# Optimization experiments

Measured on AMD Instinct MI355X. Metric: run time of the kernel, lower is better.

## Reference

```python
import jax, jax.numpy as jnp
import numpy as np

IN_F = 1024
OUT_F = 4096
BATCH = 1024

def setup_inputs() -> dict:
    key = jax.random.key(0)
    k1, k2, k3, k4 = jax.random.split(key, 4)
    s = np.sqrt(IN_F).astype(np.float32)  # weight init range, as in reset_parameters
    x = jax.random.normal(k1, (BATCH, IN_F), dtype=jnp.float32)
    weights = jax.random.uniform(k2, (OUT_F, IN_F), minval=-s, maxval=s, dtype=jnp.float32)
    centers = 0.1 * jax.random.normal(k3, (OUT_F, IN_F), dtype=jnp.float32)
    # sigmas ~ U(in-0.5, in+0.5); inv_covar = 1/sigmas
    sigmas = jax.random.uniform(k4, (OUT_F, IN_F), minval=IN_F - 0.5, maxval=IN_F + 0.5, dtype=jnp.float32)
    inv_covar = 1.0 / sigmas
    return {"x": x, "weights": weights, "centers": centers, "inv_covar": inv_covar}

def reference(x, weights, centers, inv_covar):
    # linear part with FGN bias: b_i = -sum_j W_ij * C_ij
    biases = -jnp.sum(weights * centers, axis=-1)  # (O,)
    l = x @ weights.T + biases                      # (B, O)
    # diag Mahalanobis: g_bi = sum_j (x_bj - c_ij)^2 * ic_ij^2
    # expanded to GEMMs to avoid the (B, O, I) broadcast intermediate
    ic2 = inv_covar * inv_covar                     # (O, I)
    g = ((x * x) @ ic2.T
         - 2.0 * (x @ (centers * ic2).T)
         + jnp.sum(centers * centers * ic2, axis=-1))  # (B, O)
    return l * jnp.exp(-g)
```

## Files before the change

### kernel.cpp

```cpp
#include <hip/hip_runtime.h>
#include <hip/hip_bf16.h>
#include <stdint.h>


typedef __attribute__((ext_vector_type(8))) __bf16 bf16x8;
typedef __attribute__((ext_vector_type(16))) float f32x16;

__device__ __forceinline__ unsigned short f2bf(float f) {
  union { float f; unsigned int u; } v; v.f = f;
  unsigned int u = v.u;
  unsigned int r = (u + 0x7FFFu + ((u >> 16) & 1u)) >> 16;
  return (unsigned short)r;
}

__global__ __launch_bounds__(256) void prep(
    const float* __restrict__ X, const float* __restrict__ W,
    const float* __restrict__ C, const float* __restrict__ IC,
    unsigned short* __restrict__ Wb, unsigned short* __restrict__ I2b,
    unsigned short* __restrict__ M2b,
    unsigned short* __restrict__ Xb, unsigned short* __restrict__ Qb,
    float* __restrict__ bias, float* __restrict__ dvec) {
  const int b = blockIdx.x;
  if (b < 1024) {
    const int wave = threadIdx.x >> 6;
    const int lane = threadIdx.x & 63;
    const int row  = b * 4 + wave;
    const float4* W4 = (const float4*)W + (size_t)row * 256;
    const float4* C4 = (const float4*)C + (size_t)row * 256;
    const float4* I4 = (const float4*)IC + (size_t)row * 256;
    ushort4* Wo = (ushort4*)Wb + (size_t)row * 256;
    ushort4* Io = (ushort4*)I2b + (size_t)row * 256;
    ushort4* Mo = (ushort4*)M2b + (size_t)row * 256;
    float swc = 0.f, sd = 0.f;
#pragma unroll
    for (int p = 0; p < 4; ++p) {
      int idx = lane + p * 64;
      float4 w = W4[idx], c = C4[idx], ic = I4[idx];
      float i2x = ic.x * ic.x, i2y = ic.y * ic.y, i2z = ic.z * ic.z, i2w = ic.w * ic.w;
      swc += w.x * c.x + w.y * c.y + w.z * c.z + w.w * c.w;
      sd  += c.x * c.x * i2x + c.y * c.y * i2y + c.z * c.z * i2z + c.w * c.w * i2w;
      ushort4 a, bb, m;
      a.x = f2bf(w.x); a.y = f2bf(w.y); a.z = f2bf(w.z); a.w = f2bf(w.w);
      bb.x = f2bf(i2x); bb.y = f2bf(i2y); bb.z = f2bf(i2z); bb.w = f2bf(i2w);
      m.x = f2bf(-2.f * c.x * i2x); m.y = f2bf(-2.f * c.y * i2y);
      m.z = f2bf(-2.f * c.z * i2z); m.w = f2bf(-2.f * c.w * i2w);
      Wo[idx] = a; Io[idx] = bb; Mo[idx] = m;
    }
#pragma unroll
    for (int off = 32; off > 0; off >>= 1) {
      swc += __shfl_down(swc, off);
      sd  += __shfl_down(sd, off);
    }
    if (lane == 0) { bias[row] = -swc; dvec[row] = sd; }
  } else {
    const int xb = b - 1024;
#pragma unroll
    for (int j = 0; j < 4; ++j) {
      int idx = xb * 1024 + j * 256 + threadIdx.x;
      float4 v = ((const float4*)X)[idx];
      ushort4 a, q;
      a.x = f2bf(v.x); a.y = f2bf(v.y); a.z = f2bf(v.z); a.w = f2bf(v.w);
      q.x = f2bf(v.x * v.x); q.y = f2bf(v.y * v.y);
      q.z = f2bf(v.z * v.z); q.w = f2bf(v.w * v.w);
      ((ushort4*)Xb)[idx] = a;
      ((ushort4*)Qb)[idx] = q;
    }
  }
}

#define GLD16(gp, lp)                                                          \
  __builtin_amdgcn_global_load_lds(                                            \
      (const __attribute__((address_space(1))) unsigned int*)(gp),             \
      (__attribute__((address_space(3))) unsigned int*)(lp), 16, 0, 0)

__global__ __launch_bounds__(256, 1) void fgn_gemm(
    const unsigned short* __restrict__ Xb, const unsigned short* __restrict__ Qb,
    const unsigned short* __restrict__ Wb, const unsigned short* __restrict__ I2b,
    const unsigned short* __restrict__ M2b,
    const float* __restrict__ bias, const float* __restrict__ dvec,
    float* __restrict__ out) {
  __shared__ unsigned short lds[2][5][4096];
  const int t = threadIdx.x;
  const int m0 = blockIdx.y * 128;
  const int n0 = blockIdx.x * 128;

  const int srow = t >> 2;
  const int gco  = ((t & 3) ^ ((t >> 3) & 3)) * 8;

  const unsigned short* g0 = Xb  + (size_t)(m0 + srow) * 1024 + gco;
  const unsigned short* g1 = Qb  + (size_t)(m0 + srow) * 1024 + gco;
  const unsigned short* g2 = Wb  + (size_t)(n0 + srow) * 1024 + gco;
  const unsigned short* g3 = I2b + (size_t)(n0 + srow) * 1024 + gco;
  const unsigned short* g4 = M2b + (size_t)(n0 + srow) * 1024 + gco;

#define STAGE(B, S)                                                            \
  do {                                                                         \
    const int ko = (S) * 32;                                                   \
    GLD16(g0 + ko,         &lds[B][0][t * 8]);                                 \
    GLD16(g0 + ko + 65536, &lds[B][0][2048 + t * 8]);                          \
    GLD16(g1 + ko,         &lds[B][1][t * 8]);                                 \
    GLD16(g1 + ko + 65536, &lds[B][1][2048 + t * 8]);                          \
    GLD16(g2 + ko,         &lds[B][2][t * 8]);                                 \
    GLD16(g2 + ko + 65536, &lds[B][2][2048 + t * 8]);                          \
    GLD16(g3 + ko,         &lds[B][3][t * 8]);                                 \
    GLD16(g3 + ko + 65536, &lds[B][3][2048 + t * 8]);                          \
    GLD16(g4 + ko,         &lds[B][4][t * 8]);                                 \
    GLD16(g4 + ko + 65536, &lds[B][4][2048 + t * 8]);                          \
  } while (0)

  const int wave = t >> 6, lane = t & 63;
  const int wx = wave & 1, wy = wave >> 1;
  const int ln = lane & 31, kh = lane >> 5;
  const int sw = (ln >> 1) & 3;

  int aoff[2], boff[2];
#pragma unroll
  for (int i = 0; i < 2; ++i) {
    aoff[i] = (wy * 64 + i * 32 + ln) * 32;
    boff[i] = (wx * 64 + i * 32 + ln) * 32;
  }

  f32x16 accL[2][2], accG[2][2];
#pragma unroll
  for (int i = 0; i < 2; ++i)
#pragma unroll
    for (int j = 0; j < 2; ++j) { accL[i][j] = (f32x16)0.f; accG[i][j] = (f32x16)0.f; }

#define COMPUTE(B)                                                             \
  do {                                                                         \
    _Pragma("unroll")                                                          \
    for (int ks = 0; ks < 2; ++ks) {                                           \
      const int co = ((ks * 2 + kh) ^ sw) * 8;                                 \
      bf16x8 ax[2], aq[2], bw[2], bi[2], bm[2];                                \
      _Pragma("unroll")                                                        \
      for (int i = 0; i < 2; ++i) {                                            \
        ax[i] = *(const bf16x8*)&lds[B][0][aoff[i] + co];                      \
        aq[i] = *(const bf16x8*)&lds[B][1][aoff[i] + co];                      \
        bw[i] = *(const bf16x8*)&lds[B][2][boff[i] + co];                      \
        bi[i] = *(const bf16x8*)&lds[B][3][boff[i] + co];                      \
        bm[i] = *(const bf16x8*)&lds[B][4][boff[i] + co];                      \
      }                                                                        \
      _Pragma("unroll")                                                        \
      for (int mt = 0; mt < 2; ++mt)                                           \
        _Pragma("unroll")                                                      \
        for (int nt = 0; nt < 2; ++nt) {                                       \
          accL[mt][nt] = __builtin_amdgcn_mfma_f32_32x32x16_bf16(              \
              ax[mt], bw[nt], accL[mt][nt], 0, 0, 0);                          \
          accG[mt][nt] = __builtin_amdgcn_mfma_f32_32x32x16_bf16(              \
              aq[mt], bi[nt], accG[mt][nt], 0, 0, 0);                          \
          accG[mt][nt] = __builtin_amdgcn_mfma_f32_32x32x16_bf16(              \
              ax[mt], bm[nt], accG[mt][nt], 0, 0, 0);                          \
        }                                                                      \
    }                                                                          \
  } while (0)

  STAGE(0, 0);
  __syncthreads();
#pragma unroll 1
  for (int p = 0; p < 16; ++p) {
    STAGE(1, 2 * p + 1);
    COMPUTE(0);
    __syncthreads();
    if (p < 15) STAGE(0, 2 * p + 2);
    COMPUTE(1);
    __syncthreads();
  }

#pragma unroll
  for (int nt = 0; nt < 2; ++nt) {
    int col = n0 + wx * 64 + nt * 32 + ln;
    float bn = bias[col], dn = dvec[col];
#pragma unroll
    for (int mt = 0; mt < 2; ++mt) {
      int rb = m0 + wy * 64 + mt * 32 + 4 * kh;
#pragma unroll
      for (int r = 0; r < 16; ++r) {
        int row = rb + (r & 3) + 8 * (r >> 2);
        float l  = accL[mt][nt][r] + bn;
        float gg = accG[mt][nt][r] + dn;
        out[(size_t)row * 4096 + col] = l * __expf(-gg);
      }
    }
  }
#undef STAGE
#undef COMPUTE
}

extern "C" void kernel_launch(void* const* d_in, const int* in_sizes, int n_in,
                              void* d_out, int out_size, void* d_ws, size_t ws_size,
                              hipStream_t stream) {
  const float* x  = (const float*)d_in[0];
  const float* W  = (const float*)d_in[1];
  const float* C  = (const float*)d_in[2];
  const float* IC = (const float*)d_in[3];
  float* out = (float*)d_out;

  char* ws = (char*)d_ws;
  unsigned short* Wb  = (unsigned short*)(ws);
  unsigned short* I2b = (unsigned short*)(ws + (8u << 20));
  unsigned short* M2b = (unsigned short*)(ws + (16u << 20));
  unsigned short* Xb  = (unsigned short*)(ws + (24u << 20));
  unsigned short* Qb  = (unsigned short*)(ws + (26u << 20));
  float* bias = (float*)(ws + (28u << 20));
  float* dvec = (float*)(ws + (28u << 20) + 16384);

  hipLaunchKernelGGL(prep, dim3(1280), dim3(256), 0, stream, x, W, C, IC,
                     Wb, I2b, M2b, Xb, Qb, bias, dvec);
  hipLaunchKernelGGL(fgn_gemm, dim3(32, 8), dim3(256), 0, stream,
                     Xb, Qb, Wb, I2b, M2b, bias, dvec, out);
}
```

Baseline: 138.3 us.

## Split K across wave groups, compute x² in-kernel, drop Q buffer

```diff
diff --git a/kernel.cpp b/kernel.cpp
--- a/kernel.cpp
+++ b/kernel.cpp
@@ -17,8 +17,7 @@
     const float* __restrict__ X, const float* __restrict__ W,
     const float* __restrict__ C, const float* __restrict__ IC,
     unsigned short* __restrict__ Wb, unsigned short* __restrict__ I2b,
-    unsigned short* __restrict__ M2b,
-    unsigned short* __restrict__ Xb, unsigned short* __restrict__ Qb,
+    unsigned short* __restrict__ M2b, unsigned short* __restrict__ Xb,
     float* __restrict__ bias, float* __restrict__ dvec) {
   const int b = blockIdx.x;
   if (b < 1024) {
@@ -58,12 +57,9 @@
     for (int j = 0; j < 4; ++j) {
       int idx = xb * 1024 + j * 256 + threadIdx.x;
       float4 v = ((const float4*)X)[idx];
-      ushort4 a, q;
+      ushort4 a;
       a.x = f2bf(v.x); a.y = f2bf(v.y); a.z = f2bf(v.z); a.w = f2bf(v.w);
-      q.x = f2bf(v.x * v.x); q.y = f2bf(v.y * v.y);
-      q.z = f2bf(v.z * v.z); q.w = f2bf(v.w * v.w);
       ((ushort4*)Xb)[idx] = a;
-      ((ushort4*)Qb)[idx] = q;
     }
   }
 }
@@ -73,117 +69,129 @@
       (const __attribute__((address_space(1))) unsigned int*)(gp),             \
       (__attribute__((address_space(3))) unsigned int*)(lp), 16, 0, 0)
 
-__global__ __launch_bounds__(256, 1) void fgn_gemm(
-    const unsigned short* __restrict__ Xb, const unsigned short* __restrict__ Qb,
-    const unsigned short* __restrict__ Wb, const unsigned short* __restrict__ I2b,
-    const unsigned short* __restrict__ M2b,
+__global__ __launch_bounds__(512, 2) void fgn_gemm(
+    const unsigned short* __restrict__ Xb, const unsigned short* __restrict__ Wb,
+    const unsigned short* __restrict__ I2b, const unsigned short* __restrict__ M2b,
     const float* __restrict__ bias, const float* __restrict__ dvec,
     float* __restrict__ out) {
-  __shared__ unsigned short lds[2][5][4096];
+  __shared__ unsigned char smem[65536];
+#define SBUF(B, S) ((unsigned short*)(smem + (B) * 32768 + (S) * 8192))
   const int t = threadIdx.x;
   const int m0 = blockIdx.y * 128;
   const int n0 = blockIdx.x * 128;
 
   const int srow = t >> 2;
-  const int gco  = ((t & 3) ^ ((t >> 3) & 3)) * 8;
-
-  const unsigned short* g0 = Xb  + (size_t)(m0 + srow) * 1024 + gco;
-  const unsigned short* g1 = Qb  + (size_t)(m0 + srow) * 1024 + gco;
-  const unsigned short* g2 = Wb  + (size_t)(n0 + srow) * 1024 + gco;
-  const unsigned short* g3 = I2b + (size_t)(n0 + srow) * 1024 + gco;
-  const unsigned short* g4 = M2b + (size_t)(n0 + srow) * 1024 + gco;
-
-#define STAGE(B, S)                                                            \
+  const int gco  = ((t & 3) ^ ((srow >> 1) & 3)) * 8;
+  const unsigned short* gx = Xb  + (size_t)(m0 + srow) * 1024 + gco;
+  const unsigned short* gw = Wb  + (size_t)(n0 + srow) * 1024 + gco;
+  const unsigned short* gi = I2b + (size_t)(n0 + srow) * 1024 + gco;
+  const unsigned short* gm = M2b + (size_t)(n0 + srow) * 1024 + gco;
+
+#define STAGE(B, KO)                                                           \
   do {                                                                         \
-    const int ko = (S) * 32;                                                   \
-    GLD16(g0 + ko,         &lds[B][0][t * 8]);                                 \
-    GLD16(g0 + ko + 65536, &lds[B][0][2048 + t * 8]);                          \
-    GLD16(g1 + ko,         &lds[B][1][t * 8]);                                 \
-    GLD16(g1 + ko + 65536, &lds[B][1][2048 + t * 8]);                          \
-    GLD16(g2 + ko,         &lds[B][2][t * 8]);                                 \
-    GLD16(g2 + ko + 65536, &lds[B][2][2048 + t * 8]);                          \
-    GLD16(g3 + ko,         &lds[B][3][t * 8]);                                 \
-    GLD16(g3 + ko + 65536, &lds[B][3][2048 + t * 8]);                          \
-    GLD16(g4 + ko,         &lds[B][4][t * 8]);                                 \
-    GLD16(g4 + ko + 65536, &lds[B][4][2048 + t * 8]);                          \
+    GLD16(gx + (KO), SBUF(B, 0) + t * 8);                                      \
+    GLD16(gw + (KO), SBUF(B, 1) + t * 8);                                      \
+    GLD16(gi + (KO), SBUF(B, 2) + t * 8);                                      \
+    GLD16(gm + (KO), SBUF(B, 3) + t * 8);                                      \
   } while (0)
 
-  const int wave = t >> 6, lane = t & 63;
-  const int wx = wave & 1, wy = wave >> 1;
+  const int wave = t >> 6;
+  const int kg = wave >> 2;
+  const int wq = wave & 3;
+  const int lane = t & 63;
   const int ln = lane & 31, kh = lane >> 5;
   const int sw = (ln >> 1) & 3;
-
-  int aoff[2], boff[2];
-#pragma unroll
-  for (int i = 0; i < 2; ++i) {
-    aoff[i] = (wy * 64 + i * 32 + ln) * 32;
-    boff[i] = (wx * 64 + i * 32 + ln) * 32;
-  }
-
-  f32x16 accL[2][2], accG[2][2];
-#pragma unroll
-  for (int i = 0; i < 2; ++i)
-#pragma unroll
-    for (int j = 0; j < 2; ++j) { accL[i][j] = (f32x16)0.f; accG[i][j] = (f32x16)0.f; }
+  const int co = (((kg << 1) | kh) ^ sw) * 8;
+
+  int aoff[4];
+#pragma unroll
+  for (int mt = 0; mt < 4; ++mt) aoff[mt] = (mt * 32 + ln) * 32 + co;
+  const int boff = (wq * 32 + ln) * 32 + co;
+
+  f32x16 accL[4], accG[4];
+#pragma unroll
+  for (int mt = 0; mt < 4; ++mt) { accL[mt] = (f32x16)0.f; accG[mt] = (f32x16)0.f; }
 
 #define COMPUTE(B)                                                             \
   do {                                                                         \
-    _Pragma("unroll")                                                          \
-    for (int ks = 0; ks < 2; ++ks) {                                           \
-      const int co = ((ks * 2 + kh) ^ sw) * 8;                                 \
-      bf16x8 ax[2], aq[2], bw[2], bi[2], bm[2];                                \
+    const unsigned short* p0 = SBUF(B, 0);                                     \
+    bf16x8 ax[4], aq[4];                                                       \
+    _Pragma("unroll")                                                          \
+    for (int mt = 0; mt < 4; ++mt) ax[mt] = *(const bf16x8*)(p0 + aoff[mt]);   \
+    bf16x8 bw = *(const bf16x8*)(SBUF(B, 1) + boff);                           \
+    bf16x8 bi = *(const bf16x8*)(SBUF(B, 2) + boff);                           \
+    bf16x8 bm = *(const bf16x8*)(SBUF(B, 3) + boff);                           \
+    _Pragma("unroll")                                                          \
+    for (int mt = 0; mt < 4; ++mt) {                                           \
+      bf16x8 a = ax[mt], q;                                                    \
       _Pragma("unroll")                                                        \
-      for (int i = 0; i < 2; ++i) {                                            \
-        ax[i] = *(const bf16x8*)&lds[B][0][aoff[i] + co];                      \
-        aq[i] = *(const bf16x8*)&lds[B][1][aoff[i] + co];                      \
-        bw[i] = *(const bf16x8*)&lds[B][2][boff[i] + co];                      \
-        bi[i] = *(const bf16x8*)&lds[B][3][boff[i] + co];                      \
-        bm[i] = *(const bf16x8*)&lds[B][4][boff[i] + co];                      \
-      }                                                                        \
-      _Pragma("unroll")                                                        \
-      for (int mt = 0; mt < 2; ++mt)                                           \
-        _Pragma("unroll")                                                      \
-        for (int nt = 0; nt < 2; ++nt) {                                       \
-          accL[mt][nt] = __builtin_amdgcn_mfma_f32_32x32x16_bf16(              \
-              ax[mt], bw[nt], accL[mt][nt], 0, 0, 0);                          \
-          accG[mt][nt] = __builtin_amdgcn_mfma_f32_32x32x16_bf16(              \
-              aq[mt], bi[nt], accG[mt][nt], 0, 0, 0);                          \
-          accG[mt][nt] = __builtin_amdgcn_mfma_f32_32x32x16_bf16(              \
-              ax[mt], bm[nt], accG[mt][nt], 0, 0, 0);                          \
-        }                                                                      \
+      for (int j = 0; j < 8; ++j) { float f = (float)a[j]; q[j] = (__bf16)(f * f); } \
+      aq[mt] = q;                                                              \
     }                                                                          \
+    _Pragma("unroll")                                                          \
+    for (int mt = 0; mt < 4; ++mt)                                             \
+      accL[mt] = __builtin_amdgcn_mfma_f32_32x32x16_bf16(ax[mt], bw, accL[mt], 0, 0, 0); \
+    _Pragma("unroll")                                                          \
+    for (int mt = 0; mt < 4; ++mt)                                             \
+      accG[mt] = __builtin_amdgcn_mfma_f32_32x32x16_bf16(aq[mt], bi, accG[mt], 0, 0, 0); \
+    _Pragma("unroll")                                                          \
+    for (int mt = 0; mt < 4; ++mt)                                             \
+      accG[mt] = __builtin_amdgcn_mfma_f32_32x32x16_bf16(ax[mt], bm, accG[mt], 0, 0, 0); \
   } while (0)
 
   STAGE(0, 0);
   __syncthreads();
 #pragma unroll 1
-  for (int p = 0; p < 16; ++p) {
-    STAGE(1, 2 * p + 1);
+  for (int p = 0; p < 32; p += 2) {
+    STAGE(1, (p + 1) * 32);
     COMPUTE(0);
     __syncthreads();
-    if (p < 15) STAGE(0, 2 * p + 2);
+    if (p + 2 < 32) STAGE(0, (p + 2) * 32);
     COMPUTE(1);
     __syncthreads();
   }
 
-#pragma unroll
-  for (int nt = 0; nt < 2; ++nt) {
-    int col = n0 + wx * 64 + nt * 32 + ln;
-    float bn = bias[col], dn = dvec[col];
-#pragma unroll
-    for (int mt = 0; mt < 2; ++mt) {
-      int rb = m0 + wy * 64 + mt * 32 + 4 * kh;
+  float* epi = (float*)smem;
+  const int col = n0 + wq * 32 + ln;
+  float bn = 0.f, dn = 0.f;
+  if (kg == 0) { bn = bias[col]; dn = dvec[col]; }
+
+  if (kg == 1) {
+    float* base = epi + wq * 4096 + lane * 16;
+#pragma unroll
+    for (int mt = 0; mt < 4; ++mt) *(f32x16*)(base + mt * 1024) = accL[mt];
+  }
+  __syncthreads();
+  if (kg == 0) {
+    const float* base = epi + wq * 4096 + lane * 16;
+#pragma unroll
+    for (int mt = 0; mt < 4; ++mt) accL[mt] += *(const f32x16*)(base + mt * 1024);
+  }
+  __syncthreads();
+  if (kg == 1) {
+    float* base = epi + wq * 4096 + lane * 16;
+#pragma unroll
+    for (int mt = 0; mt < 4; ++mt) *(f32x16*)(base + mt * 1024) = accG[mt];
+  }
+  __syncthreads();
+  if (kg == 0) {
+    const float* base = epi + wq * 4096 + lane * 16;
+#pragma unroll
+    for (int mt = 0; mt < 4; ++mt) {
+      accG[mt] += *(const f32x16*)(base + mt * 1024);
+      int rb = m0 + mt * 32 + 4 * kh;
 #pragma unroll
       for (int r = 0; r < 16; ++r) {
         int row = rb + (r & 3) + 8 * (r >> 2);
-        float l  = accL[mt][nt][r] + bn;
-        float gg = accG[mt][nt][r] + dn;
-        out[(size_t)row * 4096 + col] = l * __expf(-gg);
+        float l = accL[mt][r] + bn;
+        float g = accG[mt][r] + dn;
+        out[(size_t)row * 4096 + col] = l * __expf(-g);
       }
     }
   }
 #undef STAGE
 #undef COMPUTE
+#undef SBUF
 }
 
 extern "C" void kernel_launch(void* const* d_in, const int* in_sizes, int n_in,
@@ -200,12 +208,11 @@
   unsigned short* I2b = (unsigned short*)(ws + (8u << 20));
   unsigned short* M2b = (unsigned short*)(ws + (16u << 20));
   unsigned short* Xb  = (unsigned short*)(ws + (24u << 20));
-  unsigned short* Qb  = (unsigned short*)(ws + (26u << 20));
-  float* bias = (float*)(ws + (28u << 20));
-  float* dvec = (float*)(ws + (28u << 20) + 16384);
+  float* bias = (float*)(ws + (26u << 20));
+  float* dvec = (float*)(ws + (26u << 20) + 16384);
 
   hipLaunchKernelGGL(prep, dim3(1280), dim3(256), 0, stream, x, W, C, IC,
-                     Wb, I2b, M2b, Xb, Qb, bias, dvec);
-  hipLaunchKernelGGL(fgn_gemm, dim3(32, 8), dim3(256), 0, stream,
-                     Xb, Qb, Wb, I2b, M2b, bias, dvec, out);
-}
+                     Wb, I2b, M2b, Xb, bias, dvec);
+  hipLaunchKernelGGL(fgn_gemm, dim3(32, 8), dim3(512), 0, stream,
+                     Xb, Wb, I2b, M2b, bias, dvec, out);
+}
```

After: 134.6 us. 2.7% less time.
